# Performance work log

Hardware: AMD Instinct MI355X
Metric: run time of the kernel (lower is better)

The kernel has to match this reference:

```python
import jax, jax.numpy as jnp
import numpy as np

S, B, D, H, V, MF = 50, 128, 512, 512, 30000, 32
PAD = 0


def setup_inputs() -> dict:
    key = jax.random.key(0)
    ks = jax.random.split(key, 10)
    inp = {
        "user": jax.random.normal(ks[0], (B, MF), dtype=jnp.float32),
        "item": jax.random.normal(ks[1], (B, MF), dtype=jnp.float32),
        "review_input": jax.random.randint(ks[2], (S, B), 0, V, dtype=jnp.int64),
        "review_target": jax.random.randint(ks[3], (S, B), 0, V, dtype=jnp.int64),
        # learned parameters
        "word_emb": jax.random.normal(ks[4], (V, D), dtype=jnp.float32) * 0.02,
        "W_ih": jax.random.normal(ks[5], (3 * H, D), dtype=jnp.float32) * (1.0 / np.sqrt(D)),
        "W_hh": jax.random.normal(ks[6], (3 * H, H), dtype=jnp.float32) * (1.0 / np.sqrt(H)),
        "b_ih": jnp.zeros((3 * H,), dtype=jnp.float32),
        "b_hh": jnp.zeros((3 * H,), dtype=jnp.float32),
        "W_out": jax.random.normal(ks[7], (V, H), dtype=jnp.float32) * (1.0 / np.sqrt(H)),
        "b_out": jnp.zeros((V,), dtype=jnp.float32),
    }
    return inp


def _gru_forward(review_input, word_emb, W_ih, W_hh, b_ih, b_hh, W_out, b_out, batch):
    Hdim = W_hh.shape[1]
    h0 = jnp.zeros((batch, Hdim), dtype=word_emb.dtype)  # encoder returns zeros
    x = word_emb[review_input]  # [S, B, D] embedding lookup (dropout is identity in eval)

    def step(h, x_t):
        gi = x_t @ W_ih.T + b_ih            # [B, 3H]
        gh = h @ W_hh.T + b_hh              # [B, 3H]
        i_r, i_z, i_n = jnp.split(gi, 3, axis=-1)
        h_r, h_z, h_n = jnp.split(gh, 3, axis=-1)
        r = jax.nn.sigmoid(i_r + h_r)
        z = jax.nn.sigmoid(i_z + h_z)
        n = jnp.tanh(i_n + r * h_n)
        h_new = (1.0 - z) * n + z * h
        return h_new, h_new

    _, hs = jax.lax.scan(step, h0, x)       # [S, B, H]
    logits = jnp.einsum('sbh,vh->sbv', hs, W_out) + b_out  # decode from hidden_state
    return logits.reshape(-1, W_out.shape[0])  # [S*B, V], same row order as torch.cat


def reference(user, item, review_input, review_target, word_emb, W_ih, W_hh,
              b_ih, b_hh, W_out, b_out):
    batch = user.shape[0]
    logits = _gru_forward(review_input, word_emb, W_ih, W_hh, b_ih, b_hh,
                          W_out, b_out, batch)
    targets = review_target.reshape(-1)                     # [S*B]
    logp = jax.nn.log_softmax(logits, axis=-1)
    nll = -jnp.take_along_axis(logp, targets[:, None], axis=-1)[:, 0]
    mask = (targets != PAD)
    out_loss = jnp.where(mask, nll, 0.0)                    # reduction='none', ignore_index=PAD
    denom = jnp.maximum(jnp.sum(mask.astype(logits.dtype)), 1.0)
    obj = jnp.sum(out_loss) / denom                         # mean over non-pad tokens
    return (out_loss, obj)
```

## Files before the change

### kernel.cpp

```cpp
#include <hip/hip_runtime.h>
#include <hip/hip_bf16.h>

typedef __attribute__((ext_vector_type(8))) short short8;
typedef __attribute__((ext_vector_type(4))) float floatx4;

#define S_LEN  50
#define BATCH  128
#define DIM    512
#define HID    512
#define G3     1536
#define VOCAB  30000
#define TOKENS 6400
#define NB256  118
#define NVC    472
#define NWG    (25 * NB256)

#define N8_WIH   (G3 * DIM / 8)
#define N8_WHH   (G3 * HID / 8)
#define N8_WOUT  (VOCAB * DIM / 8)
#define N8_GATH  (TOKENS * DIM / 8)
#define N8_TOTAL (N8_WIH + N8_WHH + N8_WOUT + N8_GATH)

__device__ __forceinline__ float bf2f(short u) {
    union { unsigned int i; float f; } c;
    c.i = ((unsigned int)(unsigned short)u) << 16;
    return c.f;
}
__device__ __forceinline__ unsigned short f2bf(float x) {
    __hip_bfloat16 h = __float2bfloat16(x);
    unsigned short u;
    __builtin_memcpy(&u, &h, 2);
    return u;
}

__global__ void k_prep(const float* __restrict__ Wih, const float* __restrict__ Whh,
                       const float* __restrict__ Wout, const float* __restrict__ emb,
                       const int* __restrict__ idx,
                       unsigned short* __restrict__ WihB, unsigned short* __restrict__ WhhB,
                       unsigned short* __restrict__ WoutB, unsigned short* __restrict__ X) {
    int g = blockIdx.x * 256 + threadIdx.x;
    const float* src;
    unsigned short* dst;
    if (g < N8_WIH) {
        src = Wih + (size_t)g * 8;  dst = WihB + (size_t)g * 8;
    } else if (g < N8_WIH + N8_WHH) {
        int h = g - N8_WIH;
        src = Whh + (size_t)h * 8;  dst = WhhB + (size_t)h * 8;
    } else if (g < N8_WIH + N8_WHH + N8_WOUT) {
        int h = g - (N8_WIH + N8_WHH);
        src = Wout + (size_t)h * 8; dst = WoutB + (size_t)h * 8;
    } else {
        int h = g - (N8_WIH + N8_WHH + N8_WOUT);
        int token = h >> 6;
        int chunk = (h & 63) << 3;
        src = emb + (size_t)idx[token] * DIM + chunk;
        dst = X + (size_t)token * DIM + chunk;
    }
    union { short8 v; unsigned short u[8]; } o;
#pragma unroll
    for (int i = 0; i < 8; ++i) o.u[i] = f2bf(src[i]);
    *(short8*)dst = o.v;
}

__launch_bounds__(256)
__global__ void k_gemm_gi(const unsigned short* __restrict__ X,
                          const unsigned short* __restrict__ Wih,
                          const float* __restrict__ b_ih,
                          float* __restrict__ GI) {
    __shared__ unsigned short As[128 * 64];
    __shared__ unsigned short Bs[128 * 64];
    int bid = blockIdx.x;
    int wgid = (bid % 8) * 75 + bid / 8;
    int mb = wgid % 50, nb = wgid / 50;
    int m0 = mb * 128, n0 = nb * 128;

    int t = threadIdx.x, w = t >> 6, lane = t & 63;
    int wr = w >> 1, wc = w & 1;

    floatx4 zero = {0.f, 0.f, 0.f, 0.f};
    floatx4 acc[4][4];
#pragma unroll
    for (int mi = 0; mi < 4; ++mi)
#pragma unroll
        for (int ni = 0; ni < 4; ++ni) acc[mi][ni] = zero;

    int srow = t >> 1;
    int scq  = (t & 1) * 32;
    const unsigned short* gA = X   + (size_t)(m0 + srow) * DIM + scq;
    const unsigned short* gB = Wih + (size_t)(n0 + srow) * DIM + scq;
    int wo[4];
#pragma unroll
    for (int q = 0; q < 4; ++q)
        wo[q] = (srow * 128 + scq * 2 + q * 16) ^ ((srow & 7) << 4);

    for (int k0 = 0; k0 < DIM; k0 += 64) {
#pragma unroll
        for (int q = 0; q < 4; ++q) {
            *(short8*)((char*)As + wo[q]) = *(const short8*)(gA + k0 + q * 8);
            *(short8*)((char*)Bs + wo[q]) = *(const short8*)(gB + k0 + q * 8);
        }
        __syncthreads();
#pragma unroll
        for (int kt = 0; kt < 2; ++kt) {
            short8 af[4], bf[4];
#pragma unroll
            for (int mi = 0; mi < 4; ++mi) {
                int row = wr * 64 + mi * 16 + (lane & 15);
                int off = (row * 128 + kt * 64 + (lane >> 4) * 16) ^ ((row & 7) << 4);
                af[mi] = *(const short8*)((const char*)As + off);
            }
#pragma unroll
            for (int ni = 0; ni < 4; ++ni) {
                int row = wc * 64 + ni * 16 + (lane & 15);
                int off = (row * 128 + kt * 64 + (lane >> 4) * 16) ^ ((row & 7) << 4);
                bf[ni] = *(const short8*)((const char*)Bs + off);
            }
#pragma unroll
            for (int mi = 0; mi < 4; ++mi)
#pragma unroll
                for (int ni = 0; ni < 4; ++ni)
                    acc[mi][ni] = __builtin_amdgcn_mfma_f32_16x16x32_bf16(af[mi], bf[ni], acc[mi][ni], 0, 0, 0);
        }
        __syncthreads();
    }
#pragma unroll
    for (int mi = 0; mi < 4; ++mi)
#pragma unroll
        for (int ni = 0; ni < 4; ++ni) {
            int col = n0 + wc * 64 + ni * 16 + (lane & 15);
            float bo = b_ih[col];
#pragma unroll
            for (int r = 0; r < 4; ++r) {
                int row = m0 + wr * 64 + mi * 16 + (lane >> 4) * 4 + r;
                GI[(size_t)row * G3 + col] = acc[mi][ni][r] + bo;
            }
        }
}

__launch_bounds__(64)
__global__ void k_gru_step(const float* __restrict__ GI,
                           const unsigned short* __restrict__ Whh,
                           const float* __restrict__ b_hh,
                           float* __restrict__ hf,
                           const unsigned short* __restrict__ hin,
                           unsigned short* __restrict__ hout,
                           int s) {
    int lane = threadIdx.x & 63;
    int bg = blockIdx.x & 7;
    int hs = blockIdx.x >> 3;
    int jc = hs * 16 + (lane & 15);

    floatx4 acc0 = {0.f, 0.f, 0.f, 0.f};
    floatx4 acc1 = {0.f, 0.f, 0.f, 0.f};
    floatx4 acc2 = {0.f, 0.f, 0.f, 0.f};
    if (s != 0) {
        const unsigned short* pa  = hin + (size_t)(bg * 16 + (lane & 15)) * HID + (lane >> 4) * 8;
        const unsigned short* pb0 = Whh + (size_t)(0 * HID + jc) * DIM + (lane >> 4) * 8;
        const unsigned short* pb1 = Whh + (size_t)(1 * HID + jc) * DIM + (lane >> 4) * 8;
        const unsigned short* pb2 = Whh + (size_t)(2 * HID + jc) * DIM + (lane >> 4) * 8;
#pragma unroll
        for (int kt = 0; kt < 16; ++kt) {
            short8 a = *(const short8*)(pa + kt * 32);
            acc0 = __builtin_amdgcn_mfma_f32_16x16x32_bf16(a, *(const short8*)(pb0 + kt * 32), acc0, 0, 0, 0);
            acc1 = __builtin_amdgcn_mfma_f32_16x16x32_bf16(a, *(const short8*)(pb1 + kt * 32), acc1, 0, 0, 0);
            acc2 = __builtin_amdgcn_mfma_f32_16x16x32_bf16(a, *(const short8*)(pb2 + kt * 32), acc2, 0, 0, 0);
        }
    }
    float bhr = b_hh[jc], bhz = b_hh[jc + 512], bhn = b_hh[jc + 1024];
#pragma unroll
    for (int r = 0; r < 4; ++r) {
        int brow = bg * 16 + (lane >> 4) * 4 + r;
        int tok = s * BATCH + brow;
        const float* gi = GI + (size_t)tok * G3;
        float rg = 1.f / (1.f + __expf(-(gi[jc] + acc0[r] + bhr)));
        float zg = 1.f / (1.f + __expf(-(gi[jc + 512] + acc1[r] + bhz)));
        float ng = tanhf(gi[jc + 1024] + rg * (acc2[r] + bhn));
        size_t hidx = (size_t)brow * HID + jc;
        float hn = (1.f - zg) * ng + zg * hf[hidx];
        hf[hidx] = hn;
        hout[hidx] = f2bf(hn);
    }
}

__launch_bounds__(1024, 4)
__global__ void k_decode(const unsigned short* __restrict__ HS,
                         const unsigned short* __restrict__ Wout,
                         const float* __restrict__ b_out,
                         float* __restrict__ partial) {
    __shared__ unsigned short As[2][256 * 64];
    __shared__ unsigned short Bs[2][256 * 64];

    int bid = blockIdx.x;
    int xcd = bid & 7, pos = bid >> 3;
    int p = (xcd < 6 ? xcd * 369 : 2214 + (xcd - 6) * 368) + pos;
    int sgrp = p / 200;
    int rr   = p - sgrp * 200;
    int mb, nb;
    if (sgrp < 14) { mb = rr >> 3; nb = sgrp * 8 + (rr & 7); }
    else           { int q6 = rr / 6; mb = q6; nb = 112 + (rr - q6 * 6); }
    int m0 = mb * 256, n0 = nb * 256;

    int t = threadIdx.x, w = t >> 6, lane = t & 63;
    int wr = w >> 2, wc = w & 3;

    floatx4 zero = {0.f, 0.f, 0.f, 0.f};
    floatx4 acc[4][4];
#pragma unroll
    for (int mi = 0; mi < 4; ++mi)
#pragma unroll
        for (int ni = 0; ni < 4; ++ni) acc[mi][ni] = zero;

    int srow = t >> 2;
    int scb  = (t & 3) * 32;
    int swz  = (srow & 7) << 4;
    const unsigned short* gA = HS + (size_t)(m0 + srow) * DIM + (t & 3) * 16;
    int vrow = n0 + srow; if (vrow > VOCAB - 1) vrow = VOCAB - 1;
    const unsigned short* gB = Wout + (size_t)vrow * DIM + (t & 3) * 16;
    int wo0 = (srow * 128 + scb)      ^ swz;
    int wo1 = (srow * 128 + scb + 16) ^ swz;

    int roA[4][2], roB[4][2];
#pragma unroll
    for (int mi = 0; mi < 4; ++mi)
#pragma unroll
        for (int kt = 0; kt < 2; ++kt) {
            int row = wr * 64 + mi * 16 + (lane & 15);
            roA[mi][kt] = (row * 128 + kt * 64 + (lane >> 4) * 16) ^ ((row & 7) << 4);
        }
#pragma unroll
    for (int ni = 0; ni < 4; ++ni)
#pragma unroll
        for (int kt = 0; kt < 2; ++kt) {
            int row = wc * 64 + ni * 16 + (lane & 15);
            roB[ni][kt] = (row * 128 + kt * 64 + (lane >> 4) * 16) ^ ((row & 7) << 4);
        }

    {
        short8 a0 = *(const short8*)(gA);
        short8 a1 = *(const short8*)(gA + 8);
        short8 b0 = *(const short8*)(gB);
        short8 b1 = *(const short8*)(gB + 8);
        *(short8*)((char*)As[0] + wo0) = a0;
        *(short8*)((char*)As[0] + wo1) = a1;
        *(short8*)((char*)Bs[0] + wo0) = b0;
        *(short8*)((char*)Bs[0] + wo1) = b1;
    }
    __syncthreads();

    for (int ki = 0; ki < 8; ++ki) {
        int cur = ki & 1;
        short8 a0, a1, b0, b1;
        if (ki < 7) {
            int k0 = (ki + 1) * 64;
            a0 = *(const short8*)(gA + k0);
            a1 = *(const short8*)(gA + k0 + 8);
            b0 = *(const short8*)(gB + k0);
            b1 = *(const short8*)(gB + k0 + 8);
        }
#pragma unroll
        for (int kt = 0; kt < 2; ++kt) {
            short8 af[4], bf[4];
#pragma unroll
            for (int mi = 0; mi < 4; ++mi)
                af[mi] = *(const short8*)((const char*)As[cur] + roA[mi][kt]);
#pragma unroll
            for (int ni = 0; ni < 4; ++ni)
                bf[ni] = *(const short8*)((const char*)Bs[cur] + roB[ni][kt]);
#pragma unroll
            for (int mi = 0; mi < 4; ++mi)
#pragma unroll
                for (int ni = 0; ni < 4; ++ni)
                    acc[mi][ni] = __builtin_amdgcn_mfma_f32_16x16x32_bf16(af[mi], bf[ni], acc[mi][ni], 0, 0, 0);
        }
        if (ki < 7) {
            int nxt = cur ^ 1;
            *(short8*)((char*)As[nxt] + wo0) = a0;
            *(short8*)((char*)As[nxt] + wo1) = a1;
            *(short8*)((char*)Bs[nxt] + wo0) = b0;
            *(short8*)((char*)Bs[nxt] + wo1) = b1;
        }
        __syncthreads();
    }

    float esum[4][4];
#pragma unroll
    for (int mi = 0; mi < 4; ++mi)
#pragma unroll
        for (int r = 0; r < 4; ++r) esum[mi][r] = 0.f;
#pragma unroll
    for (int ni = 0; ni < 4; ++ni) {
        int v = n0 + wc * 64 + ni * 16 + (lane & 15);
        bool ok = v < VOCAB;
        float bo = ok ? b_out[v] : 0.f;
#pragma unroll
        for (int mi = 0; mi < 4; ++mi)
#pragma unroll
            for (int r = 0; r < 4; ++r) {
                float logit = acc[mi][ni][r] + bo;
                esum[mi][r] += ok ? __expf(logit) : 0.f;
            }
    }
#pragma unroll
    for (int d = 1; d < 16; d <<= 1)
#pragma unroll
        for (int mi = 0; mi < 4; ++mi)
#pragma unroll
            for (int r = 0; r < 4; ++r) esum[mi][r] += __shfl_xor(esum[mi][r], d, 64);
    if ((lane & 15) == 0) {
#pragma unroll
        for (int mi = 0; mi < 4; ++mi)
#pragma unroll
            for (int r = 0; r < 4; ++r) {
                int tok = m0 + wr * 64 + mi * 16 + (lane >> 4) * 4 + r;
                partial[(size_t)tok * 512 + nb * 4 + wc] = esum[mi][r];
            }
    }
}

__global__ void k_lse_tlg(const float* __restrict__ partial,
                          const unsigned short* __restrict__ HS,
                          const unsigned short* __restrict__ Wout,
                          const float* __restrict__ b_out,
                          const int* __restrict__ target,
                          float* __restrict__ lse, float* __restrict__ tlg) {
    int tok = blockIdx.x * 4 + (threadIdx.x >> 6);
    int lane = threadIdx.x & 63;
    int tg = target[tok];
    short8 a = *(const short8*)(HS + (size_t)tok * DIM + lane * 8);
    short8 b = *(const short8*)(Wout + (size_t)tg * DIM + lane * 8);
    float s = 0.f;
#pragma unroll
    for (int i = 0; i < 8; ++i) s += bf2f(a[i]) * bf2f(b[i]);
    float s2 = 0.f;
    for (int j = lane; j < NVC; j += 64) s2 += partial[(size_t)tok * 512 + j];
#pragma unroll
    for (int d = 1; d < 64; d <<= 1) {
        s  += __shfl_xor(s, d, 64);
        s2 += __shfl_xor(s2, d, 64);
    }
    if (lane == 0) {
        tlg[tok] = s + b_out[tg];
        lse[tok] = logf(s2);
    }
}

__global__ void k_finalize(const float* __restrict__ lse, const float* __restrict__ tlg,
                           const int* __restrict__ target, float* __restrict__ out) {
    __shared__ float ssum[256];
    __shared__ float scnt[256];
    int t = threadIdx.x;
    float ls = 0.f, lc = 0.f;
    for (int i = t; i < TOKENS; i += 256) {
        int tg = target[i];
        float loss = (tg != 0) ? (lse[i] - tlg[i]) : 0.f;
        out[i] = loss;
        ls += loss;
        lc += (tg != 0) ? 1.f : 0.f;
    }
    ssum[t] = ls; scnt[t] = lc;
    __syncthreads();
    for (int d = 128; d > 0; d >>= 1) {
        if (t < d) { ssum[t] += ssum[t + d]; scnt[t] += scnt[t + d]; }
        __syncthreads();
    }
    if (t == 0) out[TOKENS] = ssum[0] / fmaxf(scnt[0], 1.f);
}

extern "C" void kernel_launch(void* const* d_in, const int* in_sizes, int n_in,
                              void* d_out, int out_size, void* d_ws, size_t ws_size,
                              hipStream_t stream) {
    const int*   review_input  = (const int*)d_in[2];
    const int*   review_target = (const int*)d_in[3];
    const float* word_emb      = (const float*)d_in[4];
    const float* W_ih          = (const float*)d_in[5];
    const float* W_hh          = (const float*)d_in[6];
    const float* b_ih          = (const float*)d_in[7];
    const float* b_hh          = (const float*)d_in[8];
    const float* W_out         = (const float*)d_in[9];
    const float* b_out         = (const float*)d_in[10];
    float* out = (float*)d_out;

    char* ws = (char*)d_ws;
    size_t off = 0;
    auto alloc = [&](size_t n) { char* p = ws + off; off += (n + 255) & ~(size_t)255; return p; };
    unsigned short* Xb    = (unsigned short*)alloc((size_t)TOKENS * DIM * 2);
    unsigned short* Wihb  = (unsigned short*)alloc((size_t)G3 * DIM * 2);
    unsigned short* Whhb  = (unsigned short*)alloc((size_t)G3 * HID * 2);
    unsigned short* Woutb = (unsigned short*)alloc((size_t)VOCAB * DIM * 2);
    unsigned short* HS    = (unsigned short*)alloc((size_t)TOKENS * HID * 2);
    float* hf      = (float*)alloc((size_t)BATCH * HID * 4);
    float* GI      = (float*)alloc((size_t)TOKENS * G3 * 4);
    float* partial = (float*)alloc((size_t)TOKENS * 512 * 4);
    float* lse     = (float*)alloc((size_t)TOKENS * 4);
    float* tlg     = (float*)alloc((size_t)TOKENS * 4);
    (void)ws_size; (void)in_sizes; (void)n_in; (void)out_size;

    k_prep<<<dim3(N8_TOTAL / 256), dim3(256), 0, stream>>>(
        W_ih, W_hh, W_out, word_emb, review_input, Wihb, Whhb, Woutb, Xb);

    k_gemm_gi<<<dim3(600), dim3(256), 0, stream>>>(Xb, Wihb, b_ih, GI);

    hipMemsetAsync(hf, 0, (size_t)BATCH * HID * 4, stream);
    for (int s = 0; s < S_LEN; ++s) {
        const unsigned short* hin = s ? (HS + (size_t)(s - 1) * BATCH * HID) : HS;
        unsigned short* hout = HS + (size_t)s * BATCH * HID;
        k_gru_step<<<dim3(256), dim3(64), 0, stream>>>(GI, Whhb, b_hh, hf, hin, hout, s);
    }

    k_decode<<<dim3(NWG), dim3(1024), 0, stream>>>(HS, Woutb, b_out, partial);
    k_lse_tlg<<<dim3(TOKENS / 4), dim3(256), 0, stream>>>(partial, HS, Woutb, b_out, review_target, lse, tlg);
    k_finalize<<<dim3(1), dim3(256), 0, stream>>>(lse, tlg, review_target, out);
}
```

Before: 565.3 us.

## Stage output-projection GEMM tiles via direct global-to-LDS loads

The vocab-projection GEMM main loop now copies A and B tiles with global_load_lds (buffer-to-LDS DMA) instead of loading into registers and then writing to LDS. The swizzle moves to the global source column offsets so the LDS layout stays compatible with the existing fragment reads. Explicit vmcnt waits and s_barrier calls keep one stage of prefetch in flight. This removes the register staging and the ds_write instructions and frees VGPRs, at the cost of manual synchronisation whose correctness depends on the exact waitcnt counts.

```diff
diff --git a/kernel.cpp b/kernel.cpp
--- a/kernel.cpp
+++ b/kernel.cpp
@@ -31,6 +31,11 @@
     unsigned short u;
     __builtin_memcpy(&u, &h, 2);
     return u;
+}
+__device__ __forceinline__ void gl_lds16(const void* g, void* l) {
+    __builtin_amdgcn_global_load_lds(
+        (const __attribute__((address_space(1))) void*)g,
+        (__attribute__((address_space(3))) void*)l, 16, 0, 0);
 }
 
 __global__ void k_prep(const float* __restrict__ Wih, const float* __restrict__ Whh,
@@ -210,77 +215,74 @@
 #pragma unroll
         for (int ni = 0; ni < 4; ++ni) acc[mi][ni] = zero;
 
-    int srow = t >> 2;
-    int scb  = (t & 3) * 32;
-    int swz  = (srow & 7) << 4;
-    const unsigned short* gA = HS + (size_t)(m0 + srow) * DIM + (t & 3) * 16;
-    int vrow = n0 + srow; if (vrow > VOCAB - 1) vrow = VOCAB - 1;
-    const unsigned short* gB = Wout + (size_t)vrow * DIM + (t & 3) * 16;
-    int wo0 = (srow * 128 + scb)      ^ swz;
-    int wo1 = (srow * 128 + scb + 16) ^ swz;
+    int r8  = lane >> 3;
+    int cbs = ((lane & 7) ^ r8) * 16;
+    int c0 = w * 2, c1 = c0 + 1;
+    int rA0 = c0 * 8 + r8, rA1 = c1 * 8 + r8;
+    const char* gA0 = (const char*)(HS + (size_t)(m0 + rA0) * DIM) + cbs;
+    const char* gA1 = (const char*)(HS + (size_t)(m0 + rA1) * DIM) + cbs;
+    int v0 = n0 + rA0; if (v0 > VOCAB - 1) v0 = VOCAB - 1;
+    int v1 = n0 + rA1; if (v1 > VOCAB - 1) v1 = VOCAB - 1;
+    const char* gB0 = (const char*)(Wout + (size_t)v0 * DIM) + cbs;
+    const char* gB1 = (const char*)(Wout + (size_t)v1 * DIM) + cbs;
 
     int roA[4][2], roB[4][2];
 #pragma unroll
     for (int mi = 0; mi < 4; ++mi)
 #pragma unroll
-        for (int kt = 0; kt < 2; ++kt) {
+        for (int kh = 0; kh < 2; ++kh) {
             int row = wr * 64 + mi * 16 + (lane & 15);
-            roA[mi][kt] = (row * 128 + kt * 64 + (lane >> 4) * 16) ^ ((row & 7) << 4);
+            roA[mi][kh] = (row * 128 + kh * 64 + (lane >> 4) * 16) ^ ((row & 7) << 4);
         }
 #pragma unroll
     for (int ni = 0; ni < 4; ++ni)
 #pragma unroll
-        for (int kt = 0; kt < 2; ++kt) {
+        for (int kh = 0; kh < 2; ++kh) {
             int row = wc * 64 + ni * 16 + (lane & 15);
-            roB[ni][kt] = (row * 128 + kt * 64 + (lane >> 4) * 16) ^ ((row & 7) << 4);
-        }
-
-    {
-        short8 a0 = *(const short8*)(gA);
-        short8 a1 = *(const short8*)(gA + 8);
-        short8 b0 = *(const short8*)(gB);
-        short8 b1 = *(const short8*)(gB + 8);
-        *(short8*)((char*)As[0] + wo0) = a0;
-        *(short8*)((char*)As[0] + wo1) = a1;
-        *(short8*)((char*)Bs[0] + wo0) = b0;
-        *(short8*)((char*)Bs[0] + wo1) = b1;
-    }
-    __syncthreads();
-
-    for (int ki = 0; ki < 8; ++ki) {
-        int cur = ki & 1;
-        short8 a0, a1, b0, b1;
-        if (ki < 7) {
-            int k0 = (ki + 1) * 64;
-            a0 = *(const short8*)(gA + k0);
-            a1 = *(const short8*)(gA + k0 + 8);
-            b0 = *(const short8*)(gB + k0);
-            b1 = *(const short8*)(gB + k0 + 8);
-        }
-#pragma unroll
-        for (int kt = 0; kt < 2; ++kt) {
+            roB[ni][kh] = (row * 128 + kh * 64 + (lane >> 4) * 16) ^ ((row & 7) << 4);
+        }
+
+#define STAGE(kt, buf) do { int ko_ = (kt) * 128;                        \
+        gl_lds16(gA0 + ko_, (char*)As[buf] + c0 * 1024);                 \
+        gl_lds16(gA1 + ko_, (char*)As[buf] + c1 * 1024);                 \
+        gl_lds16(gB0 + ko_, (char*)Bs[buf] + c0 * 1024);                 \
+        gl_lds16(gB1 + ko_, (char*)Bs[buf] + c1 * 1024); } while (0)
+
+    STAGE(0, 0);
+    __builtin_amdgcn_sched_barrier(0);
+
+    for (int kt = 0; kt < 8; ++kt) {
+        int cur = kt & 1;
+        if (kt < 7) {
+            STAGE(kt + 1, cur ^ 1);
+            __builtin_amdgcn_sched_barrier(0);
+            asm volatile("s_waitcnt vmcnt(4)" ::: "memory");
+        } else {
+            asm volatile("s_waitcnt vmcnt(0)" ::: "memory");
+        }
+        __builtin_amdgcn_sched_barrier(0);
+        __builtin_amdgcn_s_barrier();
+        __builtin_amdgcn_sched_barrier(0);
+#pragma unroll
+        for (int kh = 0; kh < 2; ++kh) {
             short8 af[4], bf[4];
 #pragma unroll
             for (int mi = 0; mi < 4; ++mi)
-                af[mi] = *(const short8*)((const char*)As[cur] + roA[mi][kt]);
+                af[mi] = *(const short8*)((const char*)As[cur] + roA[mi][kh]);
 #pragma unroll
             for (int ni = 0; ni < 4; ++ni)
-                bf[ni] = *(const short8*)((const char*)Bs[cur] + roB[ni][kt]);
+                bf[ni] = *(const short8*)((const char*)Bs[cur] + roB[ni][kh]);
 #pragma unroll
             for (int mi = 0; mi < 4; ++mi)
 #pragma unroll
                 for (int ni = 0; ni < 4; ++ni)
                     acc[mi][ni] = __builtin_amdgcn_mfma_f32_16x16x32_bf16(af[mi], bf[ni], acc[mi][ni], 0, 0, 0);
         }
-        if (ki < 7) {
-            int nxt = cur ^ 1;
-            *(short8*)((char*)As[nxt] + wo0) = a0;
-            *(short8*)((char*)As[nxt] + wo1) = a1;
-            *(short8*)((char*)Bs[nxt] + wo0) = b0;
-            *(short8*)((char*)Bs[nxt] + wo1) = b1;
-        }
-        __syncthreads();
-    }
+        __builtin_amdgcn_sched_barrier(0);
+        __builtin_amdgcn_s_barrier();
+        __builtin_amdgcn_sched_barrier(0);
+    }
+#undef STAGE
 
     float esum[4][4];
 #pragma unroll
```

Measured after the change: 553.6 us. 1.02x faster.
